# Performance work log

Measured on AMD Instinct MI355X. Metric: run time of the kernel, lower is better.

## Reference

```python
import jax, jax.numpy as jnp
import numpy as np

INDIM = 256
NUM_CENTERS = 1024
OUTDIM = 128
N = 65536


def setup_inputs() -> dict:
    key = jax.random.key(0)
    kx, kc, kw, kb = jax.random.split(key, 4)
    x = jax.random.normal(kx, (N, INDIM), dtype=jnp.float32)
    # centers ~ U(-1, 1), sigmas = 0.1 as in init_centers_sigmas
    centers = jax.random.uniform(kc, (NUM_CENTERS, INDIM), dtype=jnp.float32, minval=-1.0, maxval=1.0)
    sigmas = jnp.full((NUM_CENTERS,), 0.1, dtype=jnp.float32)
    # nn.Linear(num_centers, outdim): weight [outdim, num_centers], bias [outdim]
    bound = 1.0 / np.sqrt(NUM_CENTERS)
    W = jax.random.uniform(kw, (OUTDIM, NUM_CENTERS), dtype=jnp.float32, minval=-bound, maxval=bound)
    b = jax.random.uniform(kb, (OUTDIM,), dtype=jnp.float32, minval=-bound, maxval=bound)
    return {"x": x, "centers": centers, "sigmas": sigmas, "W": W, "b": b}


def reference(x, centers, sigmas, W, b):
    # phi[n, m] = exp(-sigma_m * ||x_n - c_m||^2)
    x_sq = jnp.sum(x * x, axis=1)               # [N]
    c_sq = jnp.sum(centers * centers, axis=1)   # [M]
    cross = jnp.einsum('nd,md->nm', x, centers) # [N, M]
    sqdist = x_sq[:, None] + c_sq[None, :] - 2.0 * cross
    phi = jnp.exp(-sigmas[None, :] * sqdist)    # [N, M]
    return phi @ W.T + b                        # [N, outdim]
```

## Files before the change

### kernel.cpp

```cpp
#include <hip/hip_runtime.h>

typedef __attribute__((ext_vector_type(8))) short bf16x8;
typedef __attribute__((ext_vector_type(4))) float f32x4;
typedef unsigned int u32;
typedef unsigned long long u64;

#define LOG2E 1.44269504088896f

__device__ __forceinline__ short f2bf(float f) {
    union { float f; unsigned u; } v; v.f = f;
    unsigned r = v.u + 0x7fffu + ((v.u >> 16) & 1u);
    return (short)(r >> 16);
}

__device__ __forceinline__ u32 f2e4m3(float f) {
    u32 u = __float_as_uint(f);
    u32 sgn = (u >> 24) & 0x80u;
    u32 mag = u & 0x7fffffffu;
    if (mag >= 0x43E00000u) return sgn | 0x7Eu;
    if (mag < 0x3C800000u) {
        u32 q = (u32)(__uint_as_float(mag) * 512.0f + 0.5f);
        return sgn | q;
    }
    u32 r = mag + 0x0007FFFFu + ((mag >> 20) & 1u);
    u32 e8 = ((r >> 23) - 120u) & 0xFu;
    u32 m3 = (r >> 20) & 7u;
    return sgn | (e8 << 3) | m3;
}

__device__ __forceinline__ long pack8_e4m3(float4 a, float4 b) {
    u32 lo = f2e4m3(a.x) | (f2e4m3(a.y) << 8) | (f2e4m3(a.z) << 16) | (f2e4m3(a.w) << 24);
    u32 hi = f2e4m3(b.x) | (f2e4m3(b.y) << 8) | (f2e4m3(b.z) << 16) | (f2e4m3(b.w) << 24);
    return (long)(((u64)hi << 32) | lo);
}

#if __has_builtin(__builtin_amdgcn_exp2f)
#define EXP2(x) __builtin_amdgcn_exp2f(x)
#else
#define EXP2(x) __builtin_exp2f(x)
#endif

__device__ __forceinline__ u32 pack_bf16_trunc(float lo, float hi) {
#if __has_builtin(__builtin_amdgcn_perm)
    return __builtin_amdgcn_perm(__float_as_uint(hi), __float_as_uint(lo), 0x07060302u);
#else
    return (__float_as_uint(hi) & 0xFFFF0000u) | (__float_as_uint(lo) >> 16);
#endif
}

__device__ __forceinline__ void gload16(const void* g, void* l) {
    __builtin_amdgcn_global_load_lds(
        (const __attribute__((address_space(1))) void*)g,
        (__attribute__((address_space(3))) void*)l, 16, 0, 0);
}

__global__ __launch_bounds__(256) void rbf_prep(
    const float* __restrict__ centers, const float* __restrict__ sigmas,
    const float* __restrict__ W,
    char* __restrict__ cfrag8, short* __restrict__ wfrag,
    float* __restrict__ nsp, float* __restrict__ nscsp, float* __restrict__ tsp)
{
    const int tid = threadIdx.x;
    const int bid = blockIdx.x;
    if (bid < 256) {
        const int lane = tid & 63, w = tid >> 6;
        const int m = bid * 4 + w;
        const float4 v = ((const float4*)(centers + (size_t)m * 256))[lane];
        float s = v.x*v.x + v.y*v.y + v.z*v.z + v.w*v.w;
        #pragma unroll
        for (int off = 32; off >= 1; off >>= 1) s += __shfl_xor(s, off, 64);
        if (lane == 0) {
            const float sg = sigmas[m];
            const int c = m >> 5, w5 = m & 31;
            const int g = w5 >> 3, r = w5 & 7, h = r >> 2, j = r & 3;
            const int slot = ((c * 2 + h) * 4 + g) * 4 + j;
            nsp[slot]   = -sg * LOG2E;
            nscsp[slot] = -sg * s * LOG2E;
            tsp[slot]   = 2.0f * sg * LOG2E;
        }
    } else if (bid < 384) {
        const int s = (bid - 256) * 256 + tid;
        const int c = s >> 10, h = (s >> 9) & 1, ks = (s >> 6) & 7, lane = s & 63;
        const int l15 = lane & 15;
        const int m = c * 32 + 8 * (l15 >> 2) + 4 * h + (l15 & 3);
        const int k = ks * 32 + (lane >> 4) * 8;
        const float4 a = *(const float4*)(centers + (size_t)m * 256 + k);
        const float4 b = *(const float4*)(centers + (size_t)m * 256 + k + 4);
        *(long*)(cfrag8 + (size_t)s * 8) = pack8_e4m3(a, b);
    } else {
        const int s = (bid - 384) * 256 + tid;
        const int c = s >> 9, ot = (s >> 6) & 7, lane = s & 63;
        const int o = ot * 16 + (lane & 15);
        const int k = c * 32 + (lane >> 4) * 8;
        const float4 a = *(const float4*)(W + (size_t)o * 1024 + k);
        const float4 b = *(const float4*)(W + (size_t)o * 1024 + k + 4);
        bf16x8 t;
        t[0]=f2bf(a.x); t[1]=f2bf(a.y); t[2]=f2bf(a.z); t[3]=f2bf(a.w);
        t[4]=f2bf(b.x); t[5]=f2bf(b.y); t[6]=f2bf(b.z); t[7]=f2bf(b.w);
        ((bf16x8*)wfrag)[s] = t;
    }
}

__global__ __launch_bounds__(256, 2) void rbf_main(
    const float* __restrict__ x, const float* __restrict__ bvec,
    const char* __restrict__ cfrag8, const short* __restrict__ wfrag,
    const float* __restrict__ nsp, const float* __restrict__ nscsp,
    const float* __restrict__ tsp, float* __restrict__ out)
{
    __shared__ char  Cb8[4][8192];
    __shared__ short Wb[4][4096];
    __shared__ float Tls[3072];

    const int tid = threadIdx.x;
    const int lane = tid & 63;
    const int l15 = lane & 15;
    const int g4 = lane >> 4;
    const int w = tid >> 6;
    const int qb = blockIdx.x * 128 + w * 32;

#define STAGE(ci, slot) do {                                                       \
        const char* _cs = cfrag8 + (size_t)(ci) * 8192 + w * 2048 + lane * 16;     \
        gload16(_cs,        &Cb8[(slot)][w * 2048]);                               \
        gload16(_cs + 1024, &Cb8[(slot)][w * 2048 + 1024]);                        \
        const char* _ws = (const char*)wfrag + (size_t)(ci) * 8192 + w * 2048 + lane * 16; \
        gload16(_ws,        (char*)&Wb[(slot)][0] + w * 2048);                     \
        gload16(_ws + 1024, (char*)&Wb[(slot)][0] + w * 2048 + 1024);              \
    } while (0)

    STAGE(0, 0);
    STAGE(1, 1);
    STAGE(2, 2);

    ((float4*)Tls)[tid]       = ((const float4*)nsp)[tid];
    ((float4*)Tls)[256 + tid] = ((const float4*)nscsp)[tid];
    ((float4*)Tls)[512 + tid] = ((const float4*)tsp)[tid];

    long xq8[2][8];
    float xs[2];
    #pragma unroll
    for (int t = 0; t < 2; ++t) {
        const float* xr = x + (size_t)(qb + t * 16 + l15) * 256 + g4 * 8;
        float ss = 0.f;
        #pragma unroll
        for (int ks = 0; ks < 8; ++ks) {
            const float4 a = *(const float4*)(xr + ks * 32);
            const float4 b = *(const float4*)(xr + ks * 32 + 4);
            ss += a.x*a.x + a.y*a.y + a.z*a.z + a.w*a.w
                + b.x*b.x + b.y*b.y + b.z*b.z + b.w*b.w;
            xq8[t][ks] = pack8_e4m3(a, b);
        }
        ss += __shfl_xor(ss, 16, 64);
        ss += __shfl_xor(ss, 32, 64);
        xs[t] = ss;
    }

    f32x4 acc[2][8];
    #pragma unroll
    for (int t = 0; t < 2; ++t)
        #pragma unroll
        for (int ot = 0; ot < 8; ++ot) acc[t][ot] = (f32x4){0.f, 0.f, 0.f, 0.f};

    __syncthreads();

    for (int c = 0; c < 32; ++c) {
        const int slot = c & 3;
        if (c < 29) STAGE(c + 3, (c + 3) & 3);

        f32x4 s00 = (f32x4){0.f,0.f,0.f,0.f}, s01 = s00, s10 = s00, s11 = s00;
        {
            const char* cb = &Cb8[slot][0] + (size_t)lane * 8;
            __builtin_amdgcn_s_setprio(1);
            #pragma unroll
            for (int ks = 0; ks < 8; ++ks) {
                const long A0 = *(const long*)(cb + ks * 512);
                const long A1 = *(const long*)(cb + 4096 + ks * 512);
                s00 = __builtin_amdgcn_mfma_f32_16x16x32_fp8_fp8(A0, xq8[0][ks], s00, 0, 0, 0);
                s10 = __builtin_amdgcn_mfma_f32_16x16x32_fp8_fp8(A0, xq8[1][ks], s10, 0, 0, 0);
                s01 = __builtin_amdgcn_mfma_f32_16x16x32_fp8_fp8(A1, xq8[0][ks], s01, 0, 0, 0);
                s11 = __builtin_amdgcn_mfma_f32_16x16x32_fp8_fp8(A1, xq8[1][ks], s11, 0, 0, 0);
            }
            __builtin_amdgcn_s_setprio(0);
        }

        const int base0 = (c * 2 + 0) * 4 + g4;
        const int base1 = (c * 2 + 1) * 4 + g4;
        const float4 n0 = ((const float4*)Tls)[base0];
        const float4 q0 = ((const float4*)Tls)[256 + base0];
        const float4 t0 = ((const float4*)Tls)[512 + base0];
        const float4 n1 = ((const float4*)Tls)[base1];
        const float4 q1 = ((const float4*)Tls)[256 + base1];
        const float4 t1 = ((const float4*)Tls)[512 + base1];
        const float* n0p = (const float*)&n0; const float* q0p = (const float*)&q0;
        const float* t0p = (const float*)&t0; const float* n1p = (const float*)&n1;
        const float* q1p = (const float*)&q1; const float* t1p = (const float*)&t1;

        union { u32 u[4]; bf16x8 v; } pa0, pa1;
        {
            float p00[4], p01[4], p10[4], p11[4];
            #pragma unroll
            for (int j = 0; j < 4; ++j) {
                p00[j] = EXP2(fmaf(t0p[j], s00[j], fmaf(n0p[j], xs[0], q0p[j])));
                p01[j] = EXP2(fmaf(t1p[j], s01[j], fmaf(n1p[j], xs[0], q1p[j])));
                p10[j] = EXP2(fmaf(t0p[j], s10[j], fmaf(n0p[j], xs[1], q0p[j])));
                p11[j] = EXP2(fmaf(t1p[j], s11[j], fmaf(n1p[j], xs[1], q1p[j])));
            }
            pa0.u[0] = pack_bf16_trunc(p00[0], p00[1]);
            pa0.u[1] = pack_bf16_trunc(p00[2], p00[3]);
            pa0.u[2] = pack_bf16_trunc(p01[0], p01[1]);
            pa0.u[3] = pack_bf16_trunc(p01[2], p01[3]);
            pa1.u[0] = pack_bf16_trunc(p10[0], p10[1]);
            pa1.u[1] = pack_bf16_trunc(p10[2], p10[3]);
            pa1.u[2] = pack_bf16_trunc(p11[0], p11[1]);
            pa1.u[3] = pack_bf16_trunc(p11[2], p11[3]);
        }

        {
            const bf16x8* wbl = (const bf16x8*)&Wb[slot][0] + lane;
            __builtin_amdgcn_s_setprio(1);
            #pragma unroll
            for (int ot = 0; ot < 8; ++ot) {
                const bf16x8 wv = wbl[ot * 64];
                acc[0][ot] = __builtin_amdgcn_mfma_f32_16x16x32_bf16(pa0.v, wv, acc[0][ot], 0, 0, 0);
                acc[1][ot] = __builtin_amdgcn_mfma_f32_16x16x32_bf16(pa1.v, wv, acc[1][ot], 0, 0, 0);
            }
            __builtin_amdgcn_s_setprio(0);
        }

        if (c < 29)       asm volatile("s_waitcnt vmcnt(8)" ::: "memory");
        else if (c == 29) asm volatile("s_waitcnt vmcnt(4)" ::: "memory");
        else if (c == 30) asm volatile("s_waitcnt vmcnt(0)" ::: "memory");
        if (c < 31) __builtin_amdgcn_s_barrier();
    }

    #pragma unroll
    for (int t = 0; t < 2; ++t) {
        #pragma unroll
        for (int jr = 0; jr < 4; ++jr) {
            const int q = qb + t * 16 + g4 * 4 + jr;
            #pragma unroll
            for (int ot = 0; ot < 8; ++ot)
                out[(size_t)q * 128 + ot * 16 + l15] = acc[t][ot][jr] + bvec[ot * 16 + l15];
        }
    }
#undef STAGE
}

extern "C" void kernel_launch(void* const* d_in, const int* in_sizes, int n_in,
                              void* d_out, int out_size, void* d_ws, size_t ws_size,
                              hipStream_t stream) {
    (void)in_sizes; (void)n_in; (void)out_size; (void)ws_size;
    const float* x       = (const float*)d_in[0];
    const float* centers = (const float*)d_in[1];
    const float* sigmas  = (const float*)d_in[2];
    const float* W       = (const float*)d_in[3];
    const float* b       = (const float*)d_in[4];
    float* out = (float*)d_out;

    char*  cfrag8 = (char*)d_ws;
    short* wfrag  = (short*)(cfrag8 + 32768 * 8);
    float* nsp    = (float*)(wfrag + 16384 * 8);
    float* nscsp  = nsp + 1024;
    float* tsp    = nscsp + 1024;

    rbf_prep<<<448, 256, 0, stream>>>(centers, sigmas, W, cfrag8, wfrag, nsp, nscsp, tsp);
    rbf_main<<<512, 256, 0, stream>>>(x, b, cfrag8, wfrag, nsp, nscsp, tsp, out);
}
```

Before: 71.25 us.

## Software-pipeline distance MFMA chain with previous chunk's exp and output GEMM

Restructures the main loop so the FP8 distance MFMAs for chunk c are issued together with the exp, bf16 pack and output MFMAs for chunk c-1. The goal is to interleave the two MFMA streams and hide the exp/VALU latency between them. The W fragments for the previous chunk are held in registers so their LDS slot can be reused by the prefetch. The x-norm term is folded as t*(S - 0.5*|x|^2) + q, which drops the nsp table and one FMA per element. The cost is higher VGPR pressure from the extra 16 bf16x8 registers, plus an added prologue and epilogue.

```diff
diff --git a/kernel.cpp b/kernel.cpp
--- a/kernel.cpp
+++ b/kernel.cpp
@@ -107,9 +107,11 @@
     const float* __restrict__ nsp, const float* __restrict__ nscsp,
     const float* __restrict__ tsp, float* __restrict__ out)
 {
-    __shared__ char  Cb8[4][8192];
-    __shared__ short Wb[4][4096];
-    __shared__ float Tls[3072];
+    __shared__ char   Cb8[4][8192];
+    __shared__ short  Wb[4][4096];
+    __shared__ float4 Tls[512];
+
+    (void)nsp;
 
     const int tid = threadIdx.x;
     const int lane = tid & 63;
@@ -127,13 +129,58 @@
         gload16(_ws + 1024, (char*)&Wb[(slot)][0] + w * 2048 + 1024);              \
     } while (0)
 
+#define SCHAIN(sl, d00, d01, d10, d11) do {                                        \
+        const char* cb = &Cb8[(sl)][0] + (size_t)lane * 8;                         \
+        _Pragma("unroll")                                                          \
+        for (int ks = 0; ks < 8; ++ks) {                                           \
+            const long A0 = *(const long*)(cb + ks * 512);                         \
+            const long A1 = *(const long*)(cb + 4096 + ks * 512);                  \
+            d00 = __builtin_amdgcn_mfma_f32_16x16x32_fp8_fp8(A0, xq8[0][ks], d00, 0, 0, 0); \
+            d10 = __builtin_amdgcn_mfma_f32_16x16x32_fp8_fp8(A0, xq8[1][ks], d10, 0, 0, 0); \
+            d01 = __builtin_amdgcn_mfma_f32_16x16x32_fp8_fp8(A1, xq8[0][ks], d01, 0, 0, 0); \
+            d11 = __builtin_amdgcn_mfma_f32_16x16x32_fp8_fp8(A1, xq8[1][ks], d11, 0, 0, 0); \
+        }                                                                          \
+    } while (0)
+
+#define FINISH(cm) do {                                                            \
+        const int base0 = ((cm) * 2 + 0) * 4 + g4;                                 \
+        const int base1 = ((cm) * 2 + 1) * 4 + g4;                                 \
+        const float4 q0 = Tls[base0];                                              \
+        const float4 t0 = Tls[256 + base0];                                        \
+        const float4 q1 = Tls[base1];                                              \
+        const float4 t1 = Tls[256 + base1];                                        \
+        const float* q0p = (const float*)&q0; const float* t0p = (const float*)&t0;\
+        const float* q1p = (const float*)&q1; const float* t1p = (const float*)&t1;\
+        float p00[4], p01[4], p10[4], p11[4];                                      \
+        _Pragma("unroll")                                                          \
+        for (int j = 0; j < 4; ++j) {                                              \
+            p00[j] = EXP2(fmaf(t0p[j], Sp00[j] - hxs0, q0p[j]));                   \
+            p01[j] = EXP2(fmaf(t1p[j], Sp01[j] - hxs0, q1p[j]));                   \
+            p10[j] = EXP2(fmaf(t0p[j], Sp10[j] - hxs1, q0p[j]));                   \
+            p11[j] = EXP2(fmaf(t1p[j], Sp11[j] - hxs1, q1p[j]));                   \
+        }                                                                          \
+        union { u32 u[4]; bf16x8 v; } pa0, pa1;                                    \
+        pa0.u[0] = pack_bf16_trunc(p00[0], p00[1]);                                \
+        pa0.u[1] = pack_bf16_trunc(p00[2], p00[3]);                                \
+        pa0.u[2] = pack_bf16_trunc(p01[0], p01[1]);                                \
+        pa0.u[3] = pack_bf16_trunc(p01[2], p01[3]);                                \
+        pa1.u[0] = pack_bf16_trunc(p10[0], p10[1]);                                \
+        pa1.u[1] = pack_bf16_trunc(p10[2], p10[3]);                                \
+        pa1.u[2] = pack_bf16_trunc(p11[0], p11[1]);                                \
+        pa1.u[3] = pack_bf16_trunc(p11[2], p11[3]);                                \
+        _Pragma("unroll")                                                          \
+        for (int ot = 0; ot < 8; ++ot) {                                           \
+            acc[0][ot] = __builtin_amdgcn_mfma_f32_16x16x32_bf16(pa0.v, wfp[ot], acc[0][ot], 0, 0, 0); \
+            acc[1][ot] = __builtin_amdgcn_mfma_f32_16x16x32_bf16(pa1.v, wfp[ot], acc[1][ot], 0, 0, 0); \
+        }                                                                          \
+    } while (0)
+
     STAGE(0, 0);
     STAGE(1, 1);
     STAGE(2, 2);
 
-    ((float4*)Tls)[tid]       = ((const float4*)nsp)[tid];
-    ((float4*)Tls)[256 + tid] = ((const float4*)nscsp)[tid];
-    ((float4*)Tls)[512 + tid] = ((const float4*)tsp)[tid];
+    Tls[tid]       = ((const float4*)nscsp)[tid];
+    Tls[256 + tid] = ((const float4*)tsp)[tid];
 
     long xq8[2][8];
     float xs[2];
@@ -153,6 +200,8 @@
         ss += __shfl_xor(ss, 32, 64);
         xs[t] = ss;
     }
+    const float hxs0 = 0.5f * xs[0];
+    const float hxs1 = 0.5f * xs[1];
 
     f32x4 acc[2][8];
     #pragma unroll
@@ -162,75 +211,48 @@
 
     __syncthreads();
 
-    for (int c = 0; c < 32; ++c) {
+    STAGE(3, 3);
+    bf16x8 wfp[8];
+    {
+        const bf16x8* wbl = (const bf16x8*)&Wb[0][0] + lane;
+        #pragma unroll
+        for (int f = 0; f < 8; ++f) wfp[f] = wbl[f * 64];
+    }
+    f32x4 Sp00 = (f32x4){0.f,0.f,0.f,0.f}, Sp01 = Sp00, Sp10 = Sp00, Sp11 = Sp00;
+    __builtin_amdgcn_s_setprio(1);
+    SCHAIN(0, Sp00, Sp01, Sp10, Sp11);
+    __builtin_amdgcn_s_setprio(0);
+    asm volatile("s_waitcnt vmcnt(8)" ::: "memory");
+    __builtin_amdgcn_s_barrier();
+
+    for (int c = 1; c < 32; ++c) {
         const int slot = c & 3;
         if (c < 29) STAGE(c + 3, (c + 3) & 3);
 
-        f32x4 s00 = (f32x4){0.f,0.f,0.f,0.f}, s01 = s00, s10 = s00, s11 = s00;
-        {
-            const char* cb = &Cb8[slot][0] + (size_t)lane * 8;
-            __builtin_amdgcn_s_setprio(1);
-            #pragma unroll
-            for (int ks = 0; ks < 8; ++ks) {
-                const long A0 = *(const long*)(cb + ks * 512);
-                const long A1 = *(const long*)(cb + 4096 + ks * 512);
-                s00 = __builtin_amdgcn_mfma_f32_16x16x32_fp8_fp8(A0, xq8[0][ks], s00, 0, 0, 0);
-                s10 = __builtin_amdgcn_mfma_f32_16x16x32_fp8_fp8(A0, xq8[1][ks], s10, 0, 0, 0);
-                s01 = __builtin_amdgcn_mfma_f32_16x16x32_fp8_fp8(A1, xq8[0][ks], s01, 0, 0, 0);
-                s11 = __builtin_amdgcn_mfma_f32_16x16x32_fp8_fp8(A1, xq8[1][ks], s11, 0, 0, 0);
-            }
-            __builtin_amdgcn_s_setprio(0);
-        }
-
-        const int base0 = (c * 2 + 0) * 4 + g4;
-        const int base1 = (c * 2 + 1) * 4 + g4;
-        const float4 n0 = ((const float4*)Tls)[base0];
-        const float4 q0 = ((const float4*)Tls)[256 + base0];
-        const float4 t0 = ((const float4*)Tls)[512 + base0];
-        const float4 n1 = ((const float4*)Tls)[base1];
-        const float4 q1 = ((const float4*)Tls)[256 + base1];
-        const float4 t1 = ((const float4*)Tls)[512 + base1];
-        const float* n0p = (const float*)&n0; const float* q0p = (const float*)&q0;
-        const float* t0p = (const float*)&t0; const float* n1p = (const float*)&n1;
-        const float* q1p = (const float*)&q1; const float* t1p = (const float*)&t1;
-
-        union { u32 u[4]; bf16x8 v; } pa0, pa1;
-        {
-            float p00[4], p01[4], p10[4], p11[4];
-            #pragma unroll
-            for (int j = 0; j < 4; ++j) {
-                p00[j] = EXP2(fmaf(t0p[j], s00[j], fmaf(n0p[j], xs[0], q0p[j])));
-                p01[j] = EXP2(fmaf(t1p[j], s01[j], fmaf(n1p[j], xs[0], q1p[j])));
-                p10[j] = EXP2(fmaf(t0p[j], s10[j], fmaf(n0p[j], xs[1], q0p[j])));
-                p11[j] = EXP2(fmaf(t1p[j], s11[j], fmaf(n1p[j], xs[1], q1p[j])));
-            }
-            pa0.u[0] = pack_bf16_trunc(p00[0], p00[1]);
-            pa0.u[1] = pack_bf16_trunc(p00[2], p00[3]);
-            pa0.u[2] = pack_bf16_trunc(p01[0], p01[1]);
-            pa0.u[3] = pack_bf16_trunc(p01[2], p01[3]);
-            pa1.u[0] = pack_bf16_trunc(p10[0], p10[1]);
-            pa1.u[1] = pack_bf16_trunc(p10[2], p10[3]);
-            pa1.u[2] = pack_bf16_trunc(p11[0], p11[1]);
-            pa1.u[3] = pack_bf16_trunc(p11[2], p11[3]);
-        }
-
+        bf16x8 wfc[8];
         {
             const bf16x8* wbl = (const bf16x8*)&Wb[slot][0] + lane;
-            __builtin_amdgcn_s_setprio(1);
             #pragma unroll
-            for (int ot = 0; ot < 8; ++ot) {
-                const bf16x8 wv = wbl[ot * 64];
-                acc[0][ot] = __builtin_amdgcn_mfma_f32_16x16x32_bf16(pa0.v, wv, acc[0][ot], 0, 0, 0);
-                acc[1][ot] = __builtin_amdgcn_mfma_f32_16x16x32_bf16(pa1.v, wv, acc[1][ot], 0, 0, 0);
-            }
-            __builtin_amdgcn_s_setprio(0);
-        }
+            for (int f = 0; f < 8; ++f) wfc[f] = wbl[f * 64];
+        }
+
+        __builtin_amdgcn_s_setprio(1);
+        f32x4 s00 = (f32x4){0.f,0.f,0.f,0.f}, s01 = s00, s10 = s00, s11 = s00;
+        SCHAIN(slot, s00, s01, s10, s11);
+        FINISH(c - 1);
+        __builtin_amdgcn_s_setprio(0);
+
+        Sp00 = s00; Sp01 = s01; Sp10 = s10; Sp11 = s11;
+        #pragma unroll
+        for (int f = 0; f < 8; ++f) wfp[f] = wfc[f];
 
         if (c < 29)       asm volatile("s_waitcnt vmcnt(8)" ::: "memory");
         else if (c == 29) asm volatile("s_waitcnt vmcnt(4)" ::: "memory");
         else if (c == 30) asm volatile("s_waitcnt vmcnt(0)" ::: "memory");
         if (c < 31) __builtin_amdgcn_s_barrier();
     }
+
+    FINISH(31);
 
     #pragma unroll
     for (int t = 0; t < 2; ++t) {
@@ -243,6 +265,8 @@
         }
     }
 #undef STAGE
+#undef SCHAIN
+#undef FINISH
 }
 
 extern "C" void kernel_launch(void* const* d_in, const int* in_sizes, int n_in,
```

Result: no change. 70.36 us (-1.2%).
